# Optimization experiments

Measured on AMD Instinct MI355X. Metric: run time of the kernel, lower is better.

## Reference

```python
import jax, jax.numpy as jnp
import numpy as np

B, T, V, H = 1, 1024, 32000, 2048
NH, NKV, HD = 8, 4, 256
QS, KVS = NH * HD, NKV * HD
I, L = 8192, 2
SCALE = 256.0 ** -0.5          # query_pre_attn_scalar ** -0.5
ATTN_CAP, FINAL_CAP = 50.0, 30.0
WIN, EPS, THETA = 512, 1e-6, 10000.0
NEG = -2.3819763e38


def setup_inputs() -> dict:
    key = jax.random.key(0)
    ks = jax.random.split(key, 12)
    s = 0.02
    return {
        "tokens": jax.random.randint(ks[0], (B, T), 0, V, dtype=jnp.int32),
        "embed": jax.random.normal(ks[1], (V, H), jnp.float32) * s,
        "qkv_w": jax.random.normal(ks[2], (L, (NH + 2 * NKV) * HD, H), jnp.float32) * s,
        "o_w": jax.random.normal(ks[3], (L, H, NH * HD), jnp.float32) * s,
        "gate_w": jax.random.normal(ks[4], (L, I, H), jnp.float32) * s,
        "up_w": jax.random.normal(ks[5], (L, I, H), jnp.float32) * s,
        "down_w": jax.random.normal(ks[6], (L, H, I), jnp.float32) * s,
        "ln_in": jax.random.normal(ks[7], (L, H), jnp.float32) * s,   # RMSNorm weight (zeros-init offset)
        "ln_pa": jax.random.normal(ks[8], (L, H), jnp.float32) * s,
        "ln_pre": jax.random.normal(ks[9], (L, H), jnp.float32) * s,
        "ln_post": jax.random.normal(ks[10], (L, H), jnp.float32) * s,
        "ln_f": jax.random.normal(ks[11], (H,), jnp.float32) * s,
    }


def rmsnorm(x, w):
    x = x.astype(jnp.float32)
    n = x * jax.lax.rsqrt(jnp.mean(x * x, axis=-1, keepdims=True) + EPS)
    return n * (1.0 + w)  # add_unit_offset=True


def rope(x, cos, sin):
    # x: [B, T, N, HD]; split-half complex rotary as in apply_rotary_emb
    x1, x2 = jnp.split(x, 2, axis=-1)
    c = cos[None, :, None, :]
    s = sin[None, :, None, :]
    return jnp.concatenate([x1 * c - x2 * s, x1 * s + x2 * c], axis=-1)


def reference(tokens, embed, qkv_w, o_w, gate_w, up_w, down_w,
              ln_in, ln_pa, ln_pre, ln_post, ln_f):
    pos = jnp.arange(T)
    inv = 1.0 / (THETA ** (jnp.arange(0, HD, 2, dtype=jnp.float32) / HD))  # [HD/2]
    ang = pos.astype(jnp.float32)[:, None] * inv[None, :]
    cos, sin = jnp.cos(ang), jnp.sin(ang)

    i, j = pos[:, None], pos[None, :]
    causal = j <= i
    mask_global = jnp.where(causal, 0.0, NEG).astype(jnp.float32)
    mask_local = jnp.where(causal & (i - j < WIN), 0.0, NEG).astype(jnp.float32)
    masks = [mask_local, mask_global]  # layer 0: LOCAL_SLIDING, layer 1: GLOBAL

    x = embed[tokens] * jnp.sqrt(jnp.float32(H))  # Gemma embedding normalizer

    for l in range(L):
        h = rmsnorm(x, ln_in[l])
        qkv = jnp.einsum('bth,oh->bto', h, qkv_w[l])
        q = qkv[..., :QS].reshape(B, T, NH, HD)
        k = qkv[..., QS:QS + KVS].reshape(B, T, NKV, HD)
        v = qkv[..., QS + KVS:].reshape(B, T, NKV, HD)
        q = rope(q, cos, sin)
        k = rope(k, cos, sin)
        # prefill: kv_write_indices=arange(T) -> cache == current k/v
        k = jnp.repeat(k, NH // NKV, axis=2)  # GQA repeat_interleave over heads
        v = jnp.repeat(v, NH // NKV, axis=2)
        scores = jnp.einsum('bqhd,bkhd->bhqk', q * SCALE, k)
        scores = jnp.tanh(scores / ATTN_CAP) * ATTN_CAP
        scores = scores + masks[l][None, None]
        attn = jax.nn.softmax(scores.astype(jnp.float32), axis=-1)
        out = jnp.einsum('bhqk,bkhd->bqhd', attn, v).reshape(B, T, NH * HD)
        out = jnp.einsum('bto,ho->bth', out, o_w[l])
        x = x + rmsnorm(out, ln_pa[l])

        h = rmsnorm(x, ln_pre[l])
        gate = jax.nn.gelu(jnp.einsum('bth,ih->bti', h, gate_w[l]), approximate=True)
        up = jnp.einsum('bth,ih->bti', h, up_w[l])
        ff = jnp.einsum('bti,hi->bth', gate * up, down_w[l])
        x = x + rmsnorm(ff, ln_post[l])

    x = rmsnorm(x, ln_f)
    logits = jnp.einsum('bth,vh->btv', x, embed)
    logits = jnp.tanh(logits / FINAL_CAP) * FINAL_CAP  # final_logit_softcapping
    return logits
```

## Files before the change

### kernel.cpp

```cpp
#include <hip/hip_runtime.h>
#include <hip/hip_bf16.h>
#include <math.h>

typedef unsigned short u16;
typedef __attribute__((ext_vector_type(8))) short bf16x8;
typedef __attribute__((ext_vector_type(4))) float f32x4;
typedef __attribute__((ext_vector_type(4))) u16 u16x4;
typedef __attribute__((ext_vector_type(4))) unsigned u32x4;

#define T_SEQ 1024
#define HDIM  2048
#define NHEAD 8
#define NKVH  4
#define HSZ   256
#define ISZ   8192
#define NVOC  32000

#define GLDS(src, dst) __builtin_amdgcn_global_load_lds( \
    (const __attribute__((address_space(1))) void*)(src), \
    (__attribute__((address_space(3))) void*)(dst), 16, 0, 0)

__device__ __forceinline__ u16 f2bf(float f) {
    union { float f; unsigned u; } v; v.f = f;
    return (u16)((v.u + 0x7fffu + ((v.u >> 16) & 1u)) >> 16);
}
__device__ __forceinline__ float bf2f(u16 h) {
    union { unsigned u; float f; } v; v.u = (unsigned)h << 16; return v.f;
}

__device__ __forceinline__ unsigned cvt_pk_bf16(float a, float b) {
    unsigned r;
    asm("v_cvt_pk_bf16_f32 %0, %1, %2" : "=v"(r) : "v"(a), "v"(b));
    return r;
}

__device__ __forceinline__ float fast_tanh(float x) {
    float e = __expf(-2.0f * fabsf(x));
    float t = (1.0f - e) / (1.0f + e);
    return copysignf(t, x);
}

__device__ __forceinline__ f32x4 mfma16(bf16x8 a, bf16x8 b, f32x4 c) {
    return __builtin_amdgcn_mfma_f32_16x16x32_bf16(a, b, c, 0, 0, 0);
}

template<int EPI, typename CT>
__global__ __launch_bounds__(512, 1)
void gemm_f(const u16* __restrict__ A, int lda,
            const float* __restrict__ B, int ldb,
            CT* __restrict__ C, int ldc, long sC, int K,
            const float* __restrict__ UP)
{
    extern __shared__ char lds[];
    const int t = threadIdx.x;
    const int lane = t & 63, wid = t >> 6;
    const int z = blockIdx.z;
    A += (long)z * K;
    B += (long)z * K;
    C += (long)z * sC;

    const int nwg = gridDim.x * gridDim.y;
    int flat = blockIdx.y * gridDim.x + blockIdx.x;
    {
        const int q = nwg >> 3, r = nwg & 7;
        const int xcd = flat & 7, loc = flat >> 3;
        flat = (xcd < r ? xcd * (q + 1) : r * (q + 1) + (xcd - r) * q) + loc;
    }
    const int gm = gridDim.y;
    const long m0 = (long)(flat % gm) * 256;
    const long n0 = (long)(flat / gm) * 128;

    const int ar = t >> 3;
    const int asl = ((t & 7) ^ (ar & 7)) * 8;
    const u16* gA0 = A + (m0 + ar)       * (long)lda + asl;
    const u16* gA1 = A + (m0 + 64 + ar)  * (long)lda + asl;
    const u16* gA2 = A + (m0 + 128 + ar) * (long)lda + asl;
    const u16* gA3 = A + (m0 + 192 + ar) * (long)lda + asl;
    const int br = t >> 4;
    const int bsl = ((t & 15) ^ (br & 15)) * 4;
    const float* gB0 = B + (n0 + br)      * (long)ldb + bsl;
    const float* gB1 = B + (n0 + 32 + br) * (long)ldb + bsl;
    const float* gB2 = B + (n0 + 64 + br) * (long)ldb + bsl;
    const float* gB3 = B + (n0 + 96 + br) * (long)ldb + bsl;

    auto stage = [&](int kt) {
        const long ko = (long)kt * 64;
        char* d = lds + (kt & 1) * 65536 + t * 16;
        GLDS(gA0 + ko, d);
        GLDS(gA1 + ko, d + 8192);
        GLDS(gA2 + ko, d + 16384);
        GLDS(gA3 + ko, d + 24576);
        GLDS(gB0 + ko, d + 32768);
        GLDS(gB1 + ko, d + 40960);
        GLDS(gB2 + ko, d + 49152);
        GLDS(gB3 + ko, d + 57344);
    };

    f32x4 acc[4][4] = {};
    const int fr = lane & 15, kq = lane >> 4;
    const int wm = wid >> 1, wn = wid & 1;
    const int ps0 = ((kq)     ^ (fr & 7)) * 8;
    const int ps1 = ((4 + kq) ^ (fr & 7)) * 8;

    const int KT = K >> 6;
    stage(0);
    stage(1);

    for (int kt = 0; kt < KT; ++kt) {
        if (kt < KT - 1) asm volatile("s_waitcnt vmcnt(8)" ::: "memory");
        else             asm volatile("s_waitcnt vmcnt(0)" ::: "memory");
        __builtin_amdgcn_s_barrier();

        const u16*   As = (const u16*)(lds + (kt & 1) * 65536);
        const float* Bs = (const float*)(lds + (kt & 1) * 65536 + 32768);
        const int arow = wm * 64 + fr;
        const int brow = wn * 64 + fr;

        #pragma unroll
        for (int kk = 0; kk < 2; ++kk) {
            const int ps = kk ? ps1 : ps0;
            const int G = 8 * kk + 2 * kq;
            const int sa = G ^ fr, sb = (G + 1) ^ fr;
            bf16x8 af[4], bfv[4];
            #pragma unroll
            for (int mi = 0; mi < 4; ++mi)
                af[mi] = *(const bf16x8*)(As + (arow + mi * 16) * 64 + ps);
            #pragma unroll
            for (int ni = 0; ni < 4; ++ni) {
                const float* rp = Bs + (brow + ni * 16) * 64;
                f32x4 v0 = *(const f32x4*)(rp + sa * 4);
                f32x4 v1 = *(const f32x4*)(rp + sb * 4);
                u32x4 bw;
                bw.x = cvt_pk_bf16(v0.x, v0.y);
                bw.y = cvt_pk_bf16(v0.z, v0.w);
                bw.z = cvt_pk_bf16(v1.x, v1.y);
                bw.w = cvt_pk_bf16(v1.z, v1.w);
                bfv[ni] = __builtin_bit_cast(bf16x8, bw);
            }
            __builtin_amdgcn_s_setprio(1);
            #pragma unroll
            for (int mi = 0; mi < 4; ++mi)
                #pragma unroll
                for (int ni = 0; ni < 4; ++ni)
                    acc[mi][ni] = mfma16(af[mi], bfv[ni], acc[mi][ni]);
            __builtin_amdgcn_s_setprio(0);
        }
        __builtin_amdgcn_s_barrier();
        if (kt + 2 < KT) stage(kt + 2);
    }

    const int crb = kq * 4, ccol = fr;
    #pragma unroll
    for (int mi = 0; mi < 4; ++mi) {
        #pragma unroll
        for (int rr = 0; rr < 4; ++rr) {
            const long row = m0 + wm * 64 + mi * 16 + crb + rr;
            CT* cp = C + row * ldc + n0 + wn * 64 + ccol;
            #pragma unroll
            for (int ni = 0; ni < 4; ++ni) {
                float v = acc[mi][ni][rr];
                if constexpr (EPI == 1) {
                    cp[ni * 16] = (CT)(fast_tanh(v * (1.0f / 30.0f)) * 30.0f);
                } else if constexpr (EPI == 2) {
                    const float* upp = UP + row * (long)ldc + n0 + wn * 64 + ccol;
                    const float tt = fast_tanh(0.79788456f * (v + 0.044715f * v * v * v));
                    const float g = 0.5f * v * (1.0f + tt);
                    ((u16*)cp)[ni * 16] = f2bf(g * upp[ni * 16]);
                } else {
                    cp[ni * 16] = (CT)v;
                }
            }
        }
    }
}

template<int EPI, typename CT>
__global__ __launch_bounds__(256)
void gemm_bt(const u16* __restrict__ A, int lda, long sA,
             const u16* __restrict__ B, int ldb, long sB, int bshift,
             CT* __restrict__ C, int ldc, long sC, int K,
             int swin, int tflag)
{
    __shared__ u16 As[128 * 32];
    __shared__ u16 Bs[128 * 32];
    const int tid = threadIdx.x;
    const int lane = tid & 63, wid = tid >> 6;
    const int z = blockIdx.z;
    A += (long)z * sA;
    B += (long)(z >> bshift) * sB;
    C += (long)z * sC;

    const int nwg = gridDim.x * gridDim.y;
    int flat = blockIdx.y * gridDim.x + blockIdx.x;
    {
        const int q = nwg >> 3, r = nwg & 7;
        const int xcd = flat & 7, loc = flat >> 3;
        flat = (xcd < r ? xcd * (q + 1) : r * (q + 1) + (xcd - r) * q) + loc;
    }
    const int gm = gridDim.y;
    const long m0 = (long)(flat % gm) * 128;
    const long n0 = (long)(flat / gm) * 128;

    if (swin > 0) {
        if (n0 > m0 + 127) return;
        if (m0 - (n0 + 127) >= swin) return;
    }
    int klo = 0, khi = K;
    if (tflag > 0) {
        const long hi = m0 + 128;
        if (hi < khi) khi = (int)hi;
        const long lo = m0 - (long)tflag + 1;
        klo = lo > 0 ? (int)(lo & ~31L) : 0;
    }

    f32x4 acc[4][4] = {};

    const int ar = tid >> 2, ac = (tid & 3) * 8;
    const u16* gA0 = A + (m0 + ar) * lda + ac;
    const u16* gB0 = B + (n0 + ar) * (long)ldb + ac;
    const long a64 = 64L * lda, b64 = 64L * ldb;

    const int fr = lane & 15, fk = (lane >> 4) * 8;
    const int wm = (wid >> 1) * 64, wn = (wid & 1) * 64;

    for (int k0 = klo; k0 < khi; k0 += 32) {
        GLDS(gA0 + k0,       &As[tid * 8]);
        GLDS(gA0 + a64 + k0, &As[2048 + tid * 8]);
        GLDS(gB0 + k0,       &Bs[tid * 8]);
        GLDS(gB0 + b64 + k0, &Bs[2048 + tid * 8]);
        __syncthreads();
        bf16x8 af[4], bfv[4];
        #pragma unroll
        for (int mi = 0; mi < 4; ++mi)
            af[mi] = *(const bf16x8*)(&As[(wm + mi * 16 + fr) * 32 + fk]);
        #pragma unroll
        for (int ni = 0; ni < 4; ++ni)
            bfv[ni] = *(const bf16x8*)(&Bs[(wn + ni * 16 + fr) * 32 + fk]);
        #pragma unroll
        for (int mi = 0; mi < 4; ++mi)
            #pragma unroll
            for (int ni = 0; ni < 4; ++ni)
                acc[mi][ni] = mfma16(af[mi], bfv[ni], acc[mi][ni]);
        __syncthreads();
    }

    const int crb = (lane >> 4) * 4, ccol = lane & 15;
    #pragma unroll
    for (int mi = 0; mi < 4; ++mi) {
        #pragma unroll
        for (int rr = 0; rr < 4; ++rr) {
            const long row = m0 + wm + mi * 16 + crb + rr;
            CT* cp = C + row * ldc + n0 + wn + ccol;
            #pragma unroll
            for (int ni = 0; ni < 4; ++ni) {
                float v = acc[mi][ni][rr];
                if (EPI == 1) v = fast_tanh(v * (1.0f / 30.0f)) * 30.0f;
                if constexpr (sizeof(CT) == 2) cp[ni * 16] = f2bf(v);
                else                           cp[ni * 16] = v;
            }
        }
    }
}

__global__ __launch_bounds__(256)
void embed_scale(const int* __restrict__ tok, const float* __restrict__ emb,
                 float* __restrict__ x)
{
    const int t = blockIdx.x, tid = threadIdx.x;
    const long src = (long)tok[t] * HDIM;
    f32x4 a = *(const f32x4*)(emb + src + tid * 8);
    f32x4 b = *(const f32x4*)(emb + src + tid * 8 + 4);
    a *= 45.254834f; b *= 45.254834f;
    *(f32x4*)(x + (long)t * HDIM + tid * 8) = a;
    *(f32x4*)(x + (long)t * HDIM + tid * 8 + 4) = b;
}

__device__ __forceinline__ float block_sum(float v, float* red) {
    #pragma unroll
    for (int o = 32; o; o >>= 1) v += __shfl_xor(v, o);
    const int tid = threadIdx.x;
    if ((tid & 63) == 0) red[tid >> 6] = v;
    __syncthreads();
    return red[0] + red[1] + red[2] + red[3];
}

__global__ __launch_bounds__(256)
void rmsnorm_bf16(const float* __restrict__ x, const float* __restrict__ w,
                  u16* __restrict__ out)
{
    __shared__ float red[4];
    const int t = blockIdx.x, tid = threadIdx.x;
    const float* row = x + (long)t * HDIM;
    f32x4 a = *(const f32x4*)(row + tid * 8);
    f32x4 b = *(const f32x4*)(row + tid * 8 + 4);
    float ss = a.x*a.x + a.y*a.y + a.z*a.z + a.w*a.w
             + b.x*b.x + b.y*b.y + b.z*b.z + b.w*b.w;
    ss = block_sum(ss, red);
    const float r = rsqrtf(ss * (1.0f / HDIM) + 1e-6f);
    f32x4 wa = *(const f32x4*)(w + tid * 8);
    f32x4 wb = *(const f32x4*)(w + tid * 8 + 4);
    u16x4 o0, o1;
    o0.x = f2bf(a.x * r * (1.0f + wa.x)); o0.y = f2bf(a.y * r * (1.0f + wa.y));
    o0.z = f2bf(a.z * r * (1.0f + wa.z)); o0.w = f2bf(a.w * r * (1.0f + wa.w));
    o1.x = f2bf(b.x * r * (1.0f + wb.x)); o1.y = f2bf(b.y * r * (1.0f + wb.y));
    o1.z = f2bf(b.z * r * (1.0f + wb.z)); o1.w = f2bf(b.w * r * (1.0f + wb.w));
    *(u16x4*)(out + (long)t * HDIM + tid * 8) = o0;
    *(u16x4*)(out + (long)t * HDIM + tid * 8 + 4) = o1;
}

__global__ __launch_bounds__(256)
void add_rmsnorm(float* __restrict__ x, const float* __restrict__ y,
                 const float* __restrict__ w, int nsplit, long stride)
{
    __shared__ float red[4];
    const int t = blockIdx.x, tid = threadIdx.x;
    const float* yr = y + (long)t * HDIM;
    f32x4 a = *(const f32x4*)(yr + tid * 8);
    f32x4 b = *(const f32x4*)(yr + tid * 8 + 4);
    for (int s = 1; s < nsplit; ++s) {
        a += *(const f32x4*)(yr + s * stride + tid * 8);
        b += *(const f32x4*)(yr + s * stride + tid * 8 + 4);
    }
    float ss = a.x*a.x + a.y*a.y + a.z*a.z + a.w*a.w
             + b.x*b.x + b.y*b.y + b.z*b.z + b.w*b.w;
    ss = block_sum(ss, red);
    const float r = rsqrtf(ss * (1.0f / HDIM) + 1e-6f);
    f32x4 wa = *(const f32x4*)(w + tid * 8);
    f32x4 wb = *(const f32x4*)(w + tid * 8 + 4);
    float* xr = x + (long)t * HDIM;
    f32x4 xa = *(const f32x4*)(xr + tid * 8);
    f32x4 xb = *(const f32x4*)(xr + tid * 8 + 4);
    xa.x += a.x * r * (1.0f + wa.x); xa.y += a.y * r * (1.0f + wa.y);
    xa.z += a.z * r * (1.0f + wa.z); xa.w += a.w * r * (1.0f + wa.w);
    xb.x += b.x * r * (1.0f + wb.x); xb.y += b.y * r * (1.0f + wb.y);
    xb.z += b.z * r * (1.0f + wb.z); xb.w += b.w * r * (1.0f + wb.w);
    *(f32x4*)(xr + tid * 8) = xa;
    *(f32x4*)(xr + tid * 8 + 4) = xb;
}

#define QKV_STRIDE (1024L * 4096)

__global__ __launch_bounds__(256)
void qkv_post(const float* __restrict__ qkv, u16* __restrict__ qb,
              u16* __restrict__ kb)
{
    const int t = blockIdx.x, tid = threadIdx.x;
    const float* row = qkv + (long)t * 4096;
    const float ft = (float)t;
    #pragma unroll
    for (int it = 0; it < 4; ++it) {
        const int p = tid + it * 256;
        const int nh = p >> 7, d = p & 127;
        const float inv = powf(10000.0f, -(float)d * (1.0f / 128.0f));
        const float ang = ft * inv;
        const float c = cosf(ang), s = sinf(ang);
        const int i1 = nh * 256 + d, i2 = i1 + 128;
        const float x1 = row[i1] + row[i1 + QKV_STRIDE];
        const float x2 = row[i2] + row[i2 + QKV_STRIDE];
        const long ob = ((long)nh * T_SEQ + t) * HSZ;
        qb[ob + d]       = f2bf((x1 * c - x2 * s) * 0.0625f);
        qb[ob + 128 + d] = f2bf((x1 * s + x2 * c) * 0.0625f);
    }
    #pragma unroll
    for (int it = 0; it < 2; ++it) {
        const int p = tid + it * 256;
        const int kv = p >> 7, d = p & 127;
        const float inv = powf(10000.0f, -(float)d * (1.0f / 128.0f));
        const float ang = ft * inv;
        const float c = cosf(ang), s = sinf(ang);
        const int i1 = 2048 + kv * 256 + d, i2 = i1 + 128;
        const float x1 = row[i1] + row[i1 + QKV_STRIDE];
        const float x2 = row[i2] + row[i2 + QKV_STRIDE];
        const long ob = ((long)kv * T_SEQ + t) * HSZ;
        kb[ob + d]       = f2bf(x1 * c - x2 * s);
        kb[ob + 128 + d] = f2bf(x1 * s + x2 * c);
    }
}

__global__ __launch_bounds__(256)
void v_transpose(const float* __restrict__ qkvb, u16* __restrict__ vT)
{
    __shared__ u16 tile[64][65];
    const int t0 = blockIdx.x * 64, d0 = blockIdx.y * 64, kv = blockIdx.z;
    const int lane = threadIdx.x & 63, w = threadIdx.x >> 6;
    #pragma unroll
    for (int i = 0; i < 16; ++i) {
        const int t = w * 16 + i;
        const long idx = (long)(t0 + t) * 4096 + 3072 + kv * 256 + d0 + lane;
        tile[t][lane] = f2bf(qkvb[idx] + qkvb[idx + QKV_STRIDE]);
    }
    __syncthreads();
    #pragma unroll
    for (int i = 0; i < 16; ++i) {
        const int d = w * 16 + i;
        vT[((long)kv * HSZ + d0 + d) * T_SEQ + t0 + lane] = tile[lane][d];
    }
}

__global__ __launch_bounds__(256)
void softmax_mask(const float* __restrict__ sc, u16* __restrict__ pr, int win)
{
    __shared__ float redm[4], reds[4];
    const int i = blockIdx.x, h = blockIdx.y, tid = threadIdx.x;
    const long base = ((long)h * T_SEQ + i) * T_SEQ;
    f32x4 sv = *(const f32x4*)(sc + base + tid * 4);
    float vals[4];
    #pragma unroll
    for (int j = 0; j < 4; ++j) {
        const int col = tid * 4 + j;
        const float s = fast_tanh(sv[j] * 0.02f) * 50.0f;
        const bool valid = (col <= i) && ((i - col) < win);
        vals[j] = valid ? s : -3.0e38f;
    }
    float m = fmaxf(fmaxf(vals[0], vals[1]), fmaxf(vals[2], vals[3]));
    #pragma unroll
    for (int o = 32; o; o >>= 1) m = fmaxf(m, __shfl_xor(m, o));
    if ((tid & 63) == 0) redm[tid >> 6] = m;
    __syncthreads();
    m = fmaxf(fmaxf(redm[0], redm[1]), fmaxf(redm[2], redm[3]));
    float sum = 0.0f;
    #pragma unroll
    for (int j = 0; j < 4; ++j) { vals[j] = __expf(vals[j] - m); sum += vals[j]; }
    #pragma unroll
    for (int o = 32; o; o >>= 1) sum += __shfl_xor(sum, o);
    if ((tid & 63) == 0) reds[tid >> 6] = sum;
    __syncthreads();
    sum = reds[0] + reds[1] + reds[2] + reds[3];
    const float inv = 1.0f / sum;
    u16x4 o4;
    #pragma unroll
    for (int j = 0; j < 4; ++j) o4[j] = f2bf(vals[j] * inv);
    *(u16x4*)(pr + base + tid * 4) = o4;
}

extern "C" void kernel_launch(void* const* d_in, const int* in_sizes, int n_in,
                              void* d_out, int out_size, void* d_ws, size_t ws_size,
                              hipStream_t stream)
{
    (void)in_sizes; (void)n_in; (void)out_size; (void)ws_size;
    const int*   tokens = (const int*)  d_in[0];
    const float* emb    = (const float*)d_in[1];
    const float* qkv_w  = (const float*)d_in[2];
    const float* o_w    = (const float*)d_in[3];
    const float* gate_w = (const float*)d_in[4];
    const float* up_w   = (const float*)d_in[5];
    const float* down_w = (const float*)d_in[6];
    const float* ln_in  = (const float*)d_in[7];
    const float* ln_pa  = (const float*)d_in[8];
    const float* ln_pre = (const float*)d_in[9];
    const float* ln_post= (const float*)d_in[10];
    const float* ln_f   = (const float*)d_in[11];
    float* logits = (float*)d_out;

    char* base = (char*)d_ws;
    size_t off = 0;
    auto alloc = [&](size_t b) { char* p = base + off; off += (b + 255) & ~(size_t)255; return p; };

    float* x    = (float*)alloc((size_t)T_SEQ * HDIM * 4);
    u16*   hb   = (u16*)  alloc((size_t)T_SEQ * HDIM * 2);
    u16*   qb   = (u16*)  alloc((size_t)NHEAD * T_SEQ * HSZ * 2);
    u16*   kb   = (u16*)  alloc((size_t)NKVH * T_SEQ * HSZ * 2);
    u16*   vT   = (u16*)  alloc((size_t)NKVH * HSZ * T_SEQ * 2);
    u16*   ao   = (u16*)  alloc((size_t)T_SEQ * HDIM * 2);
    u16*   pb   = (u16*)  alloc((size_t)T_SEQ * ISZ * 2);
    char*  big  = alloc((size_t)2 * T_SEQ * ISZ * 4);
    float* P    = (float*)big;
    float* sc   = (float*)big;
    u16*   pr   = (u16*)(big + (size_t)NHEAD * T_SEQ * T_SEQ * 4);
    float* ub   = (float*)(big + (size_t)T_SEQ * ISZ * 4);

    const size_t LDSF = 2 * 65536;
    const long s2048 = 1024L * 2048;
    const int BIGWIN = 1 << 29;

    embed_scale<<<T_SEQ, 256, 0, stream>>>(tokens, emb, x);
    for (int l = 0; l < 2; ++l) {
        const int win = (l == 0) ? 512 : BIGWIN;
        rmsnorm_bf16<<<T_SEQ, 256, 0, stream>>>(x, ln_in + l * HDIM, hb);
        gemm_f<0, float><<<dim3(32, 4, 2), 512, LDSF, stream>>>(
            hb, HDIM, qkv_w + (size_t)l * 4096 * HDIM, HDIM, P, 4096, QKV_STRIDE, 1024, ub);
        qkv_post<<<T_SEQ, 256, 0, stream>>>(P, qb, kb);
        v_transpose<<<dim3(16, 4, 4), 256, 0, stream>>>(P, vT);
        gemm_bt<0, float><<<dim3(8, 8, NHEAD), 256, 0, stream>>>(
            qb, HSZ, (long)T_SEQ * HSZ, kb, HSZ, (long)T_SEQ * HSZ, 1,
            sc, T_SEQ, (long)T_SEQ * T_SEQ, HSZ, win, 0);
        softmax_mask<<<dim3(T_SEQ, NHEAD, 1), 256, 0, stream>>>(
            sc, pr, l == 0 ? 512 : (1 << 30));
        gemm_bt<0, u16><<<dim3(2, 8, NHEAD), 256, 0, stream>>>(
            pr, T_SEQ, (long)T_SEQ * T_SEQ, vT, T_SEQ, (long)HSZ * T_SEQ, 1,
            ao, HDIM, (long)HSZ, T_SEQ, 0, win);
        gemm_f<0, float><<<dim3(16, 4, 4), 512, LDSF, stream>>>(
            ao, HDIM, o_w + (size_t)l * HDIM * HDIM, HDIM, P, HDIM, s2048, 512, ub);
        add_rmsnorm<<<T_SEQ, 256, 0, stream>>>(x, P, ln_pa + l * HDIM, 4, s2048);
        rmsnorm_bf16<<<T_SEQ, 256, 0, stream>>>(x, ln_pre + l * HDIM, hb);
        gemm_f<0, float><<<dim3(64, 4, 1), 512, LDSF, stream>>>(
            hb, HDIM, up_w + (size_t)l * ISZ * HDIM, HDIM, ub, ISZ, 0, HDIM, ub);
        gemm_f<2, u16><<<dim3(64, 4, 1), 512, LDSF, stream>>>(
            hb, HDIM, gate_w + (size_t)l * ISZ * HDIM, HDIM, pb, ISZ, 0, HDIM, ub);
        gemm_f<0, float><<<dim3(16, 4, 4), 512, LDSF, stream>>>(
            pb, ISZ, down_w + (size_t)l * HDIM * ISZ, ISZ, P, HDIM, s2048, 2048, ub);
        add_rmsnorm<<<T_SEQ, 256, 0, stream>>>(x, P, ln_post + l * HDIM, 4, s2048);
    }
    rmsnorm_bf16<<<T_SEQ, 256, 0, stream>>>(x, ln_f, hb);
    gemm_f<1, float><<<dim3(250, 4, 1), 512, LDSF, stream>>>(
        hb, HDIM, emb, HDIM, logits, NVOC, 0, HDIM, ub);
}
```

Before: 789.4 us.

## Convert fp32 weights to bf16 once per tile via registers with triple-buffered LDS

The weight operand B is no longer copied into LDS as fp32 and converted by every wave on each read. It is now loaded into registers, converted to bf16 once, and written into LDS. The A/B staging moves from double to triple buffering with a register ping-pong so loads for tile k+2 overlap compute on tile k. This halves B's LDS footprint and removes redundant conversions. In exchange it adds register pressure, VGPR-routed global loads and more intricate waitcnt sequencing.

New measurement: 949.4 us. 1.2x slower.

```diff
diff --git a/kernel.cpp b/kernel.cpp
--- a/kernel.cpp
+++ b/kernel.cpp
@@ -46,7 +46,7 @@
 
 template<int EPI, typename CT>
 __global__ __launch_bounds__(512, 1)
-void gemm_f(const u16* __restrict__ A, int lda,
+void gemm_r(const u16* __restrict__ A, int lda,
             const float* __restrict__ B, int ldb,
             CT* __restrict__ C, int ldc, long sC, int K,
             const float* __restrict__ UP)
@@ -76,24 +76,42 @@
     const u16* gA1 = A + (m0 + 64 + ar)  * (long)lda + asl;
     const u16* gA2 = A + (m0 + 128 + ar) * (long)lda + asl;
     const u16* gA3 = A + (m0 + 192 + ar) * (long)lda + asl;
-    const int br = t >> 4;
-    const int bsl = ((t & 15) ^ (br & 15)) * 4;
-    const float* gB0 = B + (n0 + br)      * (long)ldb + bsl;
-    const float* gB1 = B + (n0 + 32 + br) * (long)ldb + bsl;
-    const float* gB2 = B + (n0 + 64 + br) * (long)ldb + bsl;
-    const float* gB3 = B + (n0 + 96 + br) * (long)ldb + bsl;
-
-    auto stage = [&](int kt) {
+
+    auto stageA = [&](int kt) {
         const long ko = (long)kt * 64;
-        char* d = lds + (kt & 1) * 65536 + t * 16;
+        char* d = lds + (kt % 3) * 49152 + t * 16;
         GLDS(gA0 + ko, d);
         GLDS(gA1 + ko, d + 8192);
         GLDS(gA2 + ko, d + 16384);
         GLDS(gA3 + ko, d + 24576);
-        GLDS(gB0 + ko, d + 32768);
-        GLDS(gB1 + ko, d + 40960);
-        GLDS(gB2 + ko, d + 49152);
-        GLDS(gB3 + ko, d + 57344);
+    };
+
+    const int bg = t & 7;
+    const float* gB = B + (n0 + (t >> 3)) * (long)ldb + bg * 8;
+    const long b64 = 64L * ldb;
+
+    auto loadB = [&](int kt, f32x4 (&R)[4]) {
+        const float* p = gB + (long)kt * 64;
+        R[0] = *(const f32x4*)(p);
+        R[1] = *(const f32x4*)(p + 4);
+        R[2] = *(const f32x4*)(p + b64);
+        R[3] = *(const f32x4*)(p + b64 + 4);
+    };
+    auto commitB = [&](int kt, f32x4 (&R)[4]) {
+        u16* bb = (u16*)(lds + (kt % 3) * 49152 + 32768);
+        const int r0 = t >> 3, r1 = 64 + (t >> 3);
+        const int sl = (bg ^ (r0 & 7)) * 8;
+        u32x4 w0, w1;
+        w0.x = cvt_pk_bf16(R[0].x, R[0].y);
+        w0.y = cvt_pk_bf16(R[0].z, R[0].w);
+        w0.z = cvt_pk_bf16(R[1].x, R[1].y);
+        w0.w = cvt_pk_bf16(R[1].z, R[1].w);
+        w1.x = cvt_pk_bf16(R[2].x, R[2].y);
+        w1.y = cvt_pk_bf16(R[2].z, R[2].w);
+        w1.z = cvt_pk_bf16(R[3].x, R[3].y);
+        w1.w = cvt_pk_bf16(R[3].z, R[3].w);
+        *(u32x4*)(bb + r0 * 64 + sl) = w0;
+        *(u32x4*)(bb + r1 * 64 + sl) = w1;
     };
 
     f32x4 acc[4][4] = {};
@@ -101,42 +119,23 @@
     const int wm = wid >> 1, wn = wid & 1;
     const int ps0 = ((kq)     ^ (fr & 7)) * 8;
     const int ps1 = ((4 + kq) ^ (fr & 7)) * 8;
-
     const int KT = K >> 6;
-    stage(0);
-    stage(1);
-
-    for (int kt = 0; kt < KT; ++kt) {
-        if (kt < KT - 1) asm volatile("s_waitcnt vmcnt(8)" ::: "memory");
-        else             asm volatile("s_waitcnt vmcnt(0)" ::: "memory");
-        __builtin_amdgcn_s_barrier();
-
-        const u16*   As = (const u16*)(lds + (kt & 1) * 65536);
-        const float* Bs = (const float*)(lds + (kt & 1) * 65536 + 32768);
+
+    auto compute = [&](int kt) {
+        const u16* As   = (const u16*)(lds + (kt % 3) * 49152);
+        const u16* Bs16 = As + 16384;
         const int arow = wm * 64 + fr;
         const int brow = wn * 64 + fr;
-
         #pragma unroll
         for (int kk = 0; kk < 2; ++kk) {
             const int ps = kk ? ps1 : ps0;
-            const int G = 8 * kk + 2 * kq;
-            const int sa = G ^ fr, sb = (G + 1) ^ fr;
             bf16x8 af[4], bfv[4];
             #pragma unroll
             for (int mi = 0; mi < 4; ++mi)
                 af[mi] = *(const bf16x8*)(As + (arow + mi * 16) * 64 + ps);
             #pragma unroll
-            for (int ni = 0; ni < 4; ++ni) {
-                const float* rp = Bs + (brow + ni * 16) * 64;
-                f32x4 v0 = *(const f32x4*)(rp + sa * 4);
-                f32x4 v1 = *(const f32x4*)(rp + sb * 4);
-                u32x4 bw;
-                bw.x = cvt_pk_bf16(v0.x, v0.y);
-                bw.y = cvt_pk_bf16(v0.z, v0.w);
-                bw.z = cvt_pk_bf16(v1.x, v1.y);
-                bw.w = cvt_pk_bf16(v1.z, v1.w);
-                bfv[ni] = __builtin_bit_cast(bf16x8, bw);
-            }
+            for (int ni = 0; ni < 4; ++ni)
+                bfv[ni] = *(const bf16x8*)(Bs16 + (brow + ni * 16) * 64 + ps);
             __builtin_amdgcn_s_setprio(1);
             #pragma unroll
             for (int mi = 0; mi < 4; ++mi)
@@ -145,8 +144,33 @@
                     acc[mi][ni] = mfma16(af[mi], bfv[ni], acc[mi][ni]);
             __builtin_amdgcn_s_setprio(0);
         }
+    };
+
+    f32x4 R0[4], R1[4];
+    loadB(0, R0);
+    stageA(0);
+    stageA(1);
+    loadB(1, R1);
+    asm volatile("s_waitcnt vmcnt(12)" ::: "memory");
+    commitB(0, R0);
+
+    auto step = [&](int kt, f32x4 (&Rld)[4], f32x4 (&Rcm)[4]) {
+        if (kt + 2 < KT) asm volatile("s_waitcnt vmcnt(8)" ::: "memory");
+        else             asm volatile("s_waitcnt vmcnt(0)" ::: "memory");
+        asm volatile("s_waitcnt lgkmcnt(0)" ::: "memory");
         __builtin_amdgcn_s_barrier();
-        if (kt + 2 < KT) stage(kt + 2);
+        if (kt + 2 < KT) { stageA(kt + 2); loadB(kt + 2, Rld); }
+        if (kt + 1 < KT) {
+            if (kt + 3 < KT) asm volatile("s_waitcnt vmcnt(8)" ::: "memory");
+            else             asm volatile("s_waitcnt vmcnt(0)" ::: "memory");
+            commitB(kt + 1, Rcm);
+        }
+        compute(kt);
+    };
+
+    for (int kt = 0; kt < KT; kt += 2) {
+        step(kt,     R0, R1);
+        step(kt + 1, R1, R0);
     }
 
     const int crb = kq * 4, ccol = fr;
@@ -469,7 +493,7 @@
     u16*   pr   = (u16*)(big + (size_t)NHEAD * T_SEQ * T_SEQ * 4);
     float* ub   = (float*)(big + (size_t)T_SEQ * ISZ * 4);
 
-    const size_t LDSF = 2 * 65536;
+    const size_t LDSR = 3 * 49152;
     const long s2048 = 1024L * 2048;
     const int BIGWIN = 1 << 29;
 
@@ -477,7 +501,7 @@
     for (int l = 0; l < 2; ++l) {
         const int win = (l == 0) ? 512 : BIGWIN;
         rmsnorm_bf16<<<T_SEQ, 256, 0, stream>>>(x, ln_in + l * HDIM, hb);
-        gemm_f<0, float><<<dim3(32, 4, 2), 512, LDSF, stream>>>(
+        gemm_r<0, float><<<dim3(32, 4, 2), 512, LDSR, stream>>>(
             hb, HDIM, qkv_w + (size_t)l * 4096 * HDIM, HDIM, P, 4096, QKV_STRIDE, 1024, ub);
         qkv_post<<<T_SEQ, 256, 0, stream>>>(P, qb, kb);
         v_transpose<<<dim3(16, 4, 4), 256, 0, stream>>>(P, vT);
@@ -489,19 +513,19 @@
         gemm_bt<0, u16><<<dim3(2, 8, NHEAD), 256, 0, stream>>>(
             pr, T_SEQ, (long)T_SEQ * T_SEQ, vT, T_SEQ, (long)HSZ * T_SEQ, 1,
             ao, HDIM, (long)HSZ, T_SEQ, 0, win);
-        gemm_f<0, float><<<dim3(16, 4, 4), 512, LDSF, stream>>>(
+        gemm_r<0, float><<<dim3(16, 4, 4), 512, LDSR, stream>>>(
             ao, HDIM, o_w + (size_t)l * HDIM * HDIM, HDIM, P, HDIM, s2048, 512, ub);
         add_rmsnorm<<<T_SEQ, 256, 0, stream>>>(x, P, ln_pa + l * HDIM, 4, s2048);
         rmsnorm_bf16<<<T_SEQ, 256, 0, stream>>>(x, ln_pre + l * HDIM, hb);
-        gemm_f<0, float><<<dim3(64, 4, 1), 512, LDSF, stream>>>(
+        gemm_r<0, float><<<dim3(64, 4, 1), 512, LDSR, stream>>>(
             hb, HDIM, up_w + (size_t)l * ISZ * HDIM, HDIM, ub, ISZ, 0, HDIM, ub);
-        gemm_f<2, u16><<<dim3(64, 4, 1), 512, LDSF, stream>>>(
+        gemm_r<2, u16><<<dim3(64, 4, 1), 512, LDSR, stream>>>(
             hb, HDIM, gate_w + (size_t)l * ISZ * HDIM, HDIM, pb, ISZ, 0, HDIM, ub);
-        gemm_f<0, float><<<dim3(16, 4, 4), 512, LDSF, stream>>>(
+        gemm_r<0, float><<<dim3(16, 4, 4), 512, LDSR, stream>>>(
             pb, ISZ, down_w + (size_t)l * HDIM * ISZ, ISZ, P, HDIM, s2048, 2048, ub);
         add_rmsnorm<<<T_SEQ, 256, 0, stream>>>(x, P, ln_post + l * HDIM, 4, s2048);
     }
     rmsnorm_bf16<<<T_SEQ, 256, 0, stream>>>(x, ln_f, hb);
-    gemm_f<1, float><<<dim3(250, 4, 1), 512, LDSF, stream>>>(
+    gemm_r<1, float><<<dim3(250, 4, 1), 512, LDSR, stream>>>(
         hb, HDIM, emb, HDIM, logits, NVOC, 0, HDIM, ub);
 }
```
